# Performance work log

Hardware: AMD Instinct MI355X
Metric: run time of the kernel (lower is better)

## Reference

```python
import jax, jax.numpy as jnp
import numpy as np
from jax import lax

LN_EPS = 1e-6  # flax LayerNorm default


def _layernorm(x, scale, bias):
    mu = jnp.mean(x, axis=-1, keepdims=True)
    var = jnp.mean(jnp.square(x - mu), axis=-1, keepdims=True)
    return (x - mu) * lax.rsqrt(var + LN_EPS) * scale + bias


def _lstm_layer(c0, h0, Wi, Wh, b, x):
    # x: [B, T, F]; carry c/h: [B, H]; gate order i, f, g, o (flax)
    def step(carry, xt):
        c, h = carry
        z = xt @ Wi + h @ Wh + b  # [B, 4H]
        i, f, g, o = jnp.split(z, 4, axis=-1)
        i = jax.nn.sigmoid(i); f = jax.nn.sigmoid(f)
        g = jnp.tanh(g); o = jax.nn.sigmoid(o)
        c = f * c + i * g
        h = o * jnp.tanh(c)
        return (c, h), h
    (cT, hT), hs = lax.scan(step, (c0, h0), jnp.swapaxes(x, 0, 1))
    return cT, hT, jnp.swapaxes(hs, 0, 1)  # hs: [B, T, H]


def setup_inputs() -> dict:
    key = jax.random.key(0)
    ks = jax.random.split(key, 16)
    B, T, F, H, P, A = 64, 128, 512, 1024, 1024, 32
    s = 0.05
    return {
        "x": jax.random.normal(ks[0], (B, T, F), jnp.float32),
        "c0": jnp.zeros((2, B, H), jnp.float32),
        "h0": jnp.zeros((2, B, H), jnp.float32),
        "W_pre": jax.random.normal(ks[1], (F, P), jnp.float32) * s,
        "b_pre": jnp.zeros((P,), jnp.float32),
        "ln_scale": jnp.ones((P,), jnp.float32),
        "ln_bias": jnp.zeros((P,), jnp.float32),
        "Wi0": jax.random.normal(ks[2], (P, 4 * H), jnp.float32) * s,
        "Wh0": jax.random.normal(ks[3], (H, 4 * H), jnp.float32) * s,
        "b0": jnp.zeros((4 * H,), jnp.float32),
        "Wi1": jax.random.normal(ks[4], (H, 4 * H), jnp.float32) * s,
        "Wh1": jax.random.normal(ks[5], (H, 4 * H), jnp.float32) * s,
        "b1": jnp.zeros((4 * H,), jnp.float32),
        "W_post": jax.random.normal(ks[6], (H, P), jnp.float32) * s,
        "b_post": jnp.zeros((P,), jnp.float32),
        "W_out": jax.random.normal(ks[7], (P, A), jnp.float32) * s,
        "b_out": jnp.zeros((A,), jnp.float32),
        "training": False,
    }


def reference(x, c0, h0, W_pre, b_pre, ln_scale, ln_bias,
              Wi0, Wh0, b0, Wi1, Wh1, b1,
              W_post, b_post, W_out, b_out, training):
    # preprocessing: Dense -> LayerNorm -> relu
    h = jax.nn.relu(_layernorm(x @ W_pre + b_pre, ln_scale, ln_bias))
    # two stacked LSTM layers scanned over time
    c1, h1, h = _lstm_layer(c0[0], h0[0], Wi0, Wh0, b0, h)
    c2, h2, h = _lstm_layer(c0[1], h0[1], Wi1, Wh1, b1, h)
    # postprocessing: Dense -> relu (dropout deterministic => identity)
    h = jax.nn.relu(h @ W_post + b_post)
    logits = h @ W_out + b_out  # [B, T, action_dim]
    new_carry = (jnp.stack([c1, c2]), jnp.stack([h1, h2]))
    return new_carry, logits
```

## Files before the change

kernel.cpp:

```cpp
#include <hip/hip_runtime.h>
#include <hip/hip_bf16.h>
#include <math.h>

typedef __attribute__((ext_vector_type(8))) short short8;
typedef __attribute__((ext_vector_type(4))) float f32x4;
typedef __attribute__((ext_vector_type(4))) unsigned u32x4;
typedef unsigned short u16;
typedef unsigned long long u64;

__device__ __forceinline__ u16 f2bf(float f) {
    union { float f; unsigned u; } v; v.f = f;
    unsigned r = v.u + 0x7fffu + ((v.u >> 16) & 1u);
    return (u16)(r >> 16);
}
__device__ __forceinline__ float bf2f(u16 b) {
    union { unsigned u; float f; } v; v.u = ((unsigned)b) << 16;
    return v.f;
}
__device__ __forceinline__ float fast_sigmoid(float x) {
    return __builtin_amdgcn_rcpf(1.f + __expf(-x));
}
__device__ __forceinline__ float fast_tanh(float x) {
    return 1.f - 2.f * __builtin_amdgcn_rcpf(1.f + __expf(2.f * x));
}
__device__ __forceinline__ u32x4 ldg16(const void* p) {
    u32x4 r;
    asm volatile("global_load_dwordx4 %0, %1, off"
                 : "=v"(r) : "v"(p) : "memory");
    return r;
}

__device__ __forceinline__ void tr_tile(const float* __restrict__ W,
                                        u16* __restrict__ WT, int K, int N,
                                        int bid, int tid, float (*tile)[33]) {
    int gx = N >> 5;
    int bx = bid % gx, by = bid / gx;
    int n0 = bx * 32, k0 = by * 32;
    int tx = tid & 31, ty = tid >> 5;
    #pragma unroll
    for (int j = 0; j < 32; j += 8)
        tile[ty + j][tx] = W[(size_t)(k0 + ty + j) * N + n0 + tx];
    __syncthreads();
    #pragma unroll
    for (int j = 0; j < 32; j += 8)
        WT[(size_t)(n0 + ty + j) * K + k0 + tx] = f2bf(tile[tx][ty + j]);
}

__global__ __launch_bounds__(256) void k_prep(
    const float* __restrict__ x, u16* __restrict__ Xb,
    const float* __restrict__ h0, u16* __restrict__ hs0, u16* __restrict__ hs1,
    unsigned* __restrict__ ctr,
    const float* __restrict__ Wpre, u16* __restrict__ WTpre,
    const float* __restrict__ Wi0, u16* __restrict__ WTi0,
    const float* __restrict__ Wh0, u16* __restrict__ WTh0,
    const float* __restrict__ Wi1, u16* __restrict__ WTi1,
    const float* __restrict__ Wh1, u16* __restrict__ WTh1,
    const float* __restrict__ Wpost, u16* __restrict__ WTpost,
    const float* __restrict__ Wout, u16* __restrict__ WTout) {
    __shared__ float tile[32][33];
    int bid = blockIdx.x, tid = threadIdx.x;
    if (bid == 0) {
        for (int i = tid; i < 4096; i += 256) ctr[i] = 0u;
        return;
    }
    bid -= 1;
    if (bid < 16384) {
        int i = bid * 256 + tid;
        Xb[i] = f2bf(x[i]);
        return;
    }
    bid -= 16384;
    if (bid < 512) {
        int i = bid * 256 + tid;
        int layer = i >> 16, j = i & 65535;
        int b = j >> 10, jj = j & 1023;
        u16 v = f2bf(h0[(size_t)layer * 65536 + j]);
        u16* dst = layer ? hs1 : hs0;
        dst[(size_t)(jj >> 3) * 512 + b * 8 + (jj & 7)] = v;
        return;
    }
    bid -= 512;
    if (bid < 512)  { tr_tile(Wpre,  WTpre,  512,  1024, bid, tid, tile); return; }
    bid -= 512;
    if (bid < 4096) { tr_tile(Wi0,   WTi0,   1024, 4096, bid, tid, tile); return; }
    bid -= 4096;
    if (bid < 4096) { tr_tile(Wh0,   WTh0,   1024, 4096, bid, tid, tile); return; }
    bid -= 4096;
    if (bid < 4096) { tr_tile(Wi1,   WTi1,   1024, 4096, bid, tid, tile); return; }
    bid -= 4096;
    if (bid < 4096) { tr_tile(Wh1,   WTh1,   1024, 4096, bid, tid, tile); return; }
    bid -= 4096;
    if (bid < 1024) { tr_tile(Wpost, WTpost, 1024, 1024, bid, tid, tile); return; }
    bid -= 1024;
    tr_tile(Wout, WTout, 1024, 32, bid, tid, tile);
}
#define PREP_BLOCKS (1 + 16384 + 512 + 512 + 4 * 4096 + 1024 + 32)

template <int MODE>
__global__ __launch_bounds__(256) void k_gemm(const u16* __restrict__ A,
                                              const u16* __restrict__ BT,
                                              const float* __restrict__ bias,
                                              void* __restrict__ Cout,
                                              int M, int N, int K) {
    const int w = threadIdx.x >> 6, l = threadIdx.x & 63;
    const int lm = l & 15, lq = l >> 4;
    const int r0 = blockIdx.y * 64 + w * 16;
    const int c0 = blockIdx.x * 64;
    const u16* arow = A + (size_t)(r0 + lm) * K + lq * 8;
    const u16* bp0 = BT + (size_t)(c0 + lm) * K + lq * 8;
    const u16* bp1 = bp0 + (size_t)16 * K;
    const u16* bp2 = bp0 + (size_t)32 * K;
    const u16* bp3 = bp0 + (size_t)48 * K;
    f32x4 acc0 = {0.f, 0.f, 0.f, 0.f}, acc1 = acc0, acc2 = acc0, acc3 = acc0;
    for (int k0 = 0; k0 < K; k0 += 32) {
        short8 a = *(const short8*)(arow + k0);
        acc0 = __builtin_amdgcn_mfma_f32_16x16x32_bf16(a, *(const short8*)(bp0 + k0), acc0, 0, 0, 0);
        acc1 = __builtin_amdgcn_mfma_f32_16x16x32_bf16(a, *(const short8*)(bp1 + k0), acc1, 0, 0, 0);
        acc2 = __builtin_amdgcn_mfma_f32_16x16x32_bf16(a, *(const short8*)(bp2 + k0), acc2, 0, 0, 0);
        acc3 = __builtin_amdgcn_mfma_f32_16x16x32_bf16(a, *(const short8*)(bp3 + k0), acc3, 0, 0, 0);
    }
    f32x4 accs[4] = {acc0, acc1, acc2, acc3};
    #pragma unroll
    for (int nt = 0; nt < 4; nt++) {
        #pragma unroll
        for (int r = 0; r < 4; r++) {
            int row = r0 + lq * 4 + r;
            int col = c0 + nt * 16 + lm;
            float v = accs[nt][r] + bias[col];
            if (MODE == 0) {
                ((float*)Cout)[(size_t)row * N + col] = v;
            } else {
                if (MODE == 2) v = fmaxf(v, 0.f);
                ((u16*)Cout)[(size_t)row * N + col] = f2bf(v);
            }
        }
    }
}

__global__ __launch_bounds__(256) void k_ln_relu(const float* __restrict__ X,
                                                 const float* __restrict__ scale,
                                                 const float* __restrict__ bias,
                                                 u16* __restrict__ preS) {
    const int N = 1024;
    int row = blockIdx.x;
    int b = row >> 7, t = row & 127;
    const float* x = X + (size_t)row * N;
    __shared__ float vbuf[1024];
    float s = 0.f, ss = 0.f;
    float vals[4];
    #pragma unroll
    for (int j = 0; j < 4; j++) {
        float v = x[threadIdx.x + 256 * j];
        vals[j] = v; s += v; ss += v * v;
    }
    #pragma unroll
    for (int o = 32; o > 0; o >>= 1) { s += __shfl_down(s, o); ss += __shfl_down(ss, o); }
    __shared__ float rs[4], rss[4];
    int w = threadIdx.x >> 6;
    if ((threadIdx.x & 63) == 0) { rs[w] = s; rss[w] = ss; }
    __syncthreads();
    __shared__ float smu, sinv;
    if (threadIdx.x == 0) {
        float a = rs[0] + rs[1] + rs[2] + rs[3];
        float bq = rss[0] + rss[1] + rss[2] + rss[3];
        float mu = a * (1.f / N);
        float var = bq * (1.f / N) - mu * mu;
        smu = mu; sinv = rsqrtf(var + 1e-6f);
    }
    __syncthreads();
    float mu = smu, inv = sinv;
    #pragma unroll
    for (int j = 0; j < 4; j++) {
        int i = threadIdx.x + 256 * j;
        float v = (vals[j] - mu) * inv * scale[i] + bias[i];
        vbuf[i] = fmaxf(v, 0.f);
    }
    __syncthreads();
    if (threadIdx.x < 128) {
        int g = threadIdx.x;
        union { u16 h[8]; u32x4 v; } pk;
        #pragma unroll
        for (int e = 0; e < 8; e++) pk.h[e] = f2bf(vbuf[g * 8 + e]);
        *(u32x4*)(preS + (size_t)t * 65536 + (size_t)g * 512 + b * 8) = pk.v;
    }
}

#define FBLOCKS 256
__global__ __launch_bounds__(512, 1) void k_lstm_fused(
    const u16* __restrict__ WiT0, const u16* __restrict__ WhT0,
    const u16* __restrict__ WiT1, const u16* __restrict__ WhT1,
    const u16* __restrict__ preS, const float* __restrict__ b0v,
    const float* __restrict__ b1v, const float* __restrict__ c0_all,
    u16* __restrict__ hs0, u16* __restrict__ hs1, u16* __restrict__ Hp,
    float* __restrict__ out, unsigned* __restrict__ ctr) {
    const int bk = blockIdx.x;
    const int role = bk >> 7;
    const int bkl = bk & 127;
    const int tid = threadIdx.x;
    const int w = tid >> 6, l = tid & 63, lm = l & 15, lq = l >> 4;
    const int kp = w >> 2, rt = w & 3;

    __shared__ u16 whs[65536];
    __shared__ float zbuf[2 * 64 * 33];
    __shared__ int gflag[2];

    {
        const u16* Wx = role ? WiT1 : WiT0;
        const u16* Wh = role ? WhT1 : WhT0;
        for (int f = tid; f < 8192; f += 512) {
            int flm = f & 15, flq = (f >> 4) & 3;
            int fi = (f >> 6) & 31;
            int rest = f >> 11;
            int fg = rest & 1, fkp = (rest >> 1) & 1;
            int lc = fg * 16 + flm;
            int gcolw = (lc >> 3) * 1024 + bkl * 8 + (lc & 7);
            int k = fi * 32 + flq * 8;
            const u16* src = (fkp == 0 ? Wx : Wh) + (size_t)gcolw * 1024 + k;
            *(short8*)(whs + (size_t)f * 8) = *(const short8*)src;
        }
    }
    if (tid == 0) { gflag[0] = -1; gflag[1] = -1; }
    const int u = tid & 7, b = tid >> 3;
    const int gcol = bkl * 8 + u;
    float c = (c0_all + (size_t)role * 65536)[(size_t)b * 1024 + gcol];
    const float* bv = role ? b1v : b0v;
    float bi0 = bv[gcol], bi1 = bv[1024 + gcol];
    float bi2 = bv[2048 + gcol], bi3 = bv[3072 + gcol];
    u16* hs_my = role ? hs1 : hs0;
    float* c_out = out + (size_t)role * 65536;
    float* h_out = out + 131072 + (size_t)role * 65536;
    const int lanoff = (lq * 16 + lm) * 8;
    __syncthreads();

    for (int t = 0; t < 128; t++) {
        if (role || kp == 1) {
            int need = (role && kp == 0) ? t + 1 : t;
            if (rt == 0) {
                if (need > 0) {
                    int cbase = (role && kp) ? 128 : 0;
                    for (;;) {
                        unsigned a0 = __hip_atomic_load(&ctr[(cbase + l) * 16], __ATOMIC_RELAXED,
                                                        __HIP_MEMORY_SCOPE_AGENT);
                        unsigned a1 = __hip_atomic_load(&ctr[(cbase + 64 + l) * 16], __ATOMIC_RELAXED,
                                                        __HIP_MEMORY_SCOPE_AGENT);
                        if (__all((a0 >= (unsigned)need) && (a1 >= (unsigned)need))) break;
                        __builtin_amdgcn_s_sleep(1);
                    }
                }
                __hip_atomic_store(&gflag[kp], need, __ATOMIC_RELAXED,
                                   __HIP_MEMORY_SCOPE_WORKGROUP);
            } else {
                while (__hip_atomic_load(&gflag[kp], __ATOMIC_RELAXED,
                                         __HIP_MEMORY_SCOPE_WORKGROUP) < need)
                    __builtin_amdgcn_s_sleep(1);
            }
        }

        const u16* abase;
        if (!role) abase = (kp == 0) ? preS + (size_t)t * 65536
                                     : hs0 + (size_t)t * 65536;
        else       abase = (kp == 0) ? hs0 + (size_t)(t + 1) * 65536
                                     : hs1 + (size_t)t * 65536;
        const u16* arow = abase + (size_t)lq * 512 + (rt * 16 + lm) * 8;
        const u16* bw0 = whs + kp * 32768 + lanoff;

        f32x4 zv = {0.f, 0.f, 0.f, 0.f};
        f32x4 ac0[4] = {zv, zv, zv, zv}, ac1[4] = {zv, zv, zv, zv};
        #define STEPF(Ai, i)                                                      \
        {   union { u32x4 q; short8 v; } _a; _a.q = (Ai);                         \
            short8 _b0 = *(const short8*)(bw0 + (i) * 512);                       \
            short8 _b1 = *(const short8*)(bw0 + 16384 + (i) * 512);               \
            ac0[(i) & 3] = __builtin_amdgcn_mfma_f32_16x16x32_bf16(_a.v, _b0, ac0[(i) & 3], 0, 0, 0); \
            ac1[(i) & 3] = __builtin_amdgcn_mfma_f32_16x16x32_bf16(_a.v, _b1, ac1[(i) & 3], 0, 0, 0); }

        u32x4 A0 = ldg16(arow +     0), A1 = ldg16(arow +  2048);
        u32x4 A2 = ldg16(arow +  4096), A3 = ldg16(arow +  6144);
        u32x4 A4 = ldg16(arow +  8192), A5 = ldg16(arow + 10240);
        u32x4 A6 = ldg16(arow + 12288), A7 = ldg16(arow + 14336);
        u32x4 A8 = ldg16(arow + 16384), A9 = ldg16(arow + 18432);
        u32x4 A10 = ldg16(arow + 20480), A11 = ldg16(arow + 22528);
        u32x4 A12 = ldg16(arow + 24576), A13 = ldg16(arow + 26624);
        u32x4 A14 = ldg16(arow + 28672), A15 = ldg16(arow + 30720);
        u32x4 A16 = ldg16(arow + 32768), A17 = ldg16(arow + 34816);
        u32x4 A18 = ldg16(arow + 36864), A19 = ldg16(arow + 38912);
        u32x4 A20 = ldg16(arow + 40960), A21 = ldg16(arow + 43008);
        u32x4 A22 = ldg16(arow + 45056), A23 = ldg16(arow + 47104);
        u32x4 A24 = ldg16(arow + 49152), A25 = ldg16(arow + 51200);
        u32x4 A26 = ldg16(arow + 53248), A27 = ldg16(arow + 55296);
        u32x4 A28 = ldg16(arow + 57344), A29 = ldg16(arow + 59392);
        u32x4 A30 = ldg16(arow + 61440), A31 = ldg16(arow + 63488);
        asm volatile("s_waitcnt vmcnt(24)"
                     : "+v"(A0), "+v"(A1), "+v"(A2), "+v"(A3),
                       "+v"(A4), "+v"(A5), "+v"(A6), "+v"(A7) :: "memory");
        STEPF(A0, 0) STEPF(A1, 1) STEPF(A2, 2) STEPF(A3, 3)
        STEPF(A4, 4) STEPF(A5, 5) STEPF(A6, 6) STEPF(A7, 7)
        asm volatile("s_waitcnt vmcnt(16)"
                     : "+v"(A8), "+v"(A9), "+v"(A10), "+v"(A11),
                       "+v"(A12), "+v"(A13), "+v"(A14), "+v"(A15) :: "memory");
        STEPF(A8, 8) STEPF(A9, 9) STEPF(A10, 10) STEPF(A11, 11)
        STEPF(A12, 12) STEPF(A13, 13) STEPF(A14, 14) STEPF(A15, 15)
        asm volatile("s_waitcnt vmcnt(8)"
                     : "+v"(A16), "+v"(A17), "+v"(A18), "+v"(A19),
                       "+v"(A20), "+v"(A21), "+v"(A22), "+v"(A23) :: "memory");
        STEPF(A16, 16) STEPF(A17, 17) STEPF(A18, 18) STEPF(A19, 19)
        STEPF(A20, 20) STEPF(A21, 21) STEPF(A22, 22) STEPF(A23, 23)
        asm volatile("s_waitcnt vmcnt(0)"
                     : "+v"(A24), "+v"(A25), "+v"(A26), "+v"(A27),
                       "+v"(A28), "+v"(A29), "+v"(A30), "+v"(A31) :: "memory");
        STEPF(A24, 24) STEPF(A25, 25) STEPF(A26, 26) STEPF(A27, 27)
        STEPF(A28, 28) STEPF(A29, 29) STEPF(A30, 30) STEPF(A31, 31)
        #undef STEPF
        f32x4 acc0 = (ac0[0] + ac0[1]) + (ac0[2] + ac0[3]);
        f32x4 acc1 = (ac1[0] + ac1[1]) + (ac1[2] + ac1[3]);

        {
            float* zb = zbuf + (size_t)kp * 2112;
            #pragma unroll
            for (int r = 0; r < 4; r++) {
                int row = rt * 16 + lq * 4 + r;
                zb[row * 33 + lm] = acc0[r];
                zb[row * 33 + 16 + lm] = acc1[r];
            }
        }
        __syncthreads();

        {
            const float* z0 = zbuf + (size_t)b * 33;
            const float* z1 = z0 + 2112;
            float gi = z0[u]      + z1[u]      + bi0;
            float gf = z0[8 + u]  + z1[8 + u]  + bi1;
            float gg = z0[16 + u] + z1[16 + u] + bi2;
            float go = z0[24 + u] + z1[24 + u] + bi3;
            gi = fast_sigmoid(gi);
            gf = fast_sigmoid(gf);
            gg = fast_tanh(gg);
            go = fast_sigmoid(go);
            c = gf * c + gi * gg;
            float h = go * fast_tanh(c);
            unsigned hv = (unsigned)f2bf(h);
            int base = l & 56;
            unsigned p0 = __shfl(hv, base + 0, 64) | (__shfl(hv, base + 1, 64) << 16);
            unsigned p1 = __shfl(hv, base + 2, 64) | (__shfl(hv, base + 3, 64) << 16);
            unsigned p2 = __shfl(hv, base + 4, 64) | (__shfl(hv, base + 5, 64) << 16);
            unsigned p3 = __shfl(hv, base + 6, 64) | (__shfl(hv, base + 7, 64) << 16);
            if (u == 0) {
                u32x4 pv = {p0, p1, p2, p3};
                u16* dst = hs_my + (size_t)(t + 1) * 65536 + (size_t)bkl * 512 + b * 8;
                asm volatile("global_store_dwordx4 %0, %1, off sc0 sc1"
                             :: "v"(dst), "v"(pv) : "memory");
                if (role) {
                    u16* d2 = Hp + (size_t)(t * 64 + b) * 1024 + bkl * 8;
                    *(u32x4*)d2 = pv;
                }
            }
            if (t == 127) {
                c_out[(size_t)b * 1024 + gcol] = c;
                h_out[(size_t)b * 1024 + gcol] = h;
            }
        }
        __syncthreads();

        if (tid == 0)
            __hip_atomic_store(&ctr[bk * 16], (unsigned)(t + 1), __ATOMIC_RELAXED,
                               __HIP_MEMORY_SCOPE_AGENT);
    }
}

__global__ __launch_bounds__(256) void k_logits(const u16* __restrict__ Pact,
                                                const u16* __restrict__ WoT,
                                                const float* __restrict__ bout,
                                                float* __restrict__ out) {
    int r = blockIdx.x * 8 + (threadIdx.x >> 5);
    int n = threadIdx.x & 31;
    const u16* a = Pact + (size_t)r * 1024;
    const u16* wv = WoT + (size_t)n * 1024;
    float s = 0.f;
    for (int k = 0; k < 1024; k += 8) {
        short8 av = *(const short8*)(a + k);
        short8 wvv = *(const short8*)(wv + k);
        #pragma unroll
        for (int j = 0; j < 8; j++)
            s += bf2f((u16)av[j]) * bf2f((u16)wvv[j]);
    }
    int t = r >> 6, b = r & 63;
    out[((size_t)b * 128 + t) * 32 + n] = s + bout[n];
}

extern "C" void kernel_launch(void* const* d_in, const int* in_sizes, int n_in,
                              void* d_out, int out_size, void* d_ws, size_t ws_size,
                              hipStream_t stream) {
    const float* x      = (const float*)d_in[0];
    const float* c0     = (const float*)d_in[1];
    const float* h0     = (const float*)d_in[2];
    const float* W_pre  = (const float*)d_in[3];
    const float* b_pre  = (const float*)d_in[4];
    const float* ln_s   = (const float*)d_in[5];
    const float* ln_b   = (const float*)d_in[6];
    const float* Wi0    = (const float*)d_in[7];
    const float* Wh0    = (const float*)d_in[8];
    const float* b0     = (const float*)d_in[9];
    const float* Wi1    = (const float*)d_in[10];
    const float* Wh1    = (const float*)d_in[11];
    const float* b1     = (const float*)d_in[12];
    const float* W_post = (const float*)d_in[13];
    const float* b_post = (const float*)d_in[14];
    const float* W_out  = (const float*)d_in[15];
    const float* b_out  = (const float*)d_in[16];
    float* out = (float*)d_out;

    char* ws = (char*)d_ws;
    size_t off = 0;
    auto alloc = [&](size_t bytes) {
        void* p = ws + off;
        off += (bytes + 255) & ~(size_t)255;
        return p;
    };
    u16* WTpre  = (u16*)alloc((size_t)1024 * 512 * 2);
    u16* WTi0   = (u16*)alloc((size_t)4096 * 1024 * 2);
    u16* WTh0   = (u16*)alloc((size_t)4096 * 1024 * 2);
    u16* WTi1   = (u16*)alloc((size_t)4096 * 1024 * 2);
    u16* WTh1   = (u16*)alloc((size_t)4096 * 1024 * 2);
    u16* WTpost = (u16*)alloc((size_t)1024 * 1024 * 2);
    u16* WTout  = (u16*)alloc((size_t)32 * 1024 * 2);
    u16* Xb     = (u16*)alloc((size_t)8192 * 512 * 2);
    u16* preS   = (u16*)alloc((size_t)128 * 65536 * 2);
    u16* hs0    = (u16*)alloc((size_t)129 * 65536 * 2);
    u16* hs1    = (u16*)alloc((size_t)129 * 65536 * 2);
    u16* postact= (u16*)alloc((size_t)8192 * 1024 * 2);
    unsigned* ctr = (unsigned*)alloc(32768);
    void* unionreg = alloc((size_t)8192 * 4096 * 2);
    float* pre_f32 = (float*)unionreg;
    u16* Hplain = (u16*)unionreg;

    k_prep<<<PREP_BLOCKS, 256, 0, stream>>>(
        x, Xb, h0, hs0, hs1, ctr,
        W_pre, WTpre, Wi0, WTi0, Wh0, WTh0, Wi1, WTi1, Wh1, WTh1,
        W_post, WTpost, W_out, WTout);

    k_gemm<0><<<dim3(16, 128), 256, 0, stream>>>(Xb, WTpre, b_pre, pre_f32, 8192, 1024, 512);
    k_ln_relu<<<8192, 256, 0, stream>>>(pre_f32, ln_s, ln_b, preS);

    {
        const u16* WiT0_ = WTi0; const u16* WhT0_ = WTh0;
        const u16* WiT1_ = WTi1; const u16* WhT1_ = WTh1;
        const u16* preS_ = preS; const float* b0_ = b0; const float* b1_ = b1;
        const float* c0_ = c0; u16* hs0_ = hs0; u16* hs1_ = hs1;
        u16* Hp_ = Hplain; float* out_ = out; unsigned* ctr_ = ctr;
        void* args[] = {&WiT0_, &WhT0_, &WiT1_, &WhT1_, &preS_, &b0_, &b1_,
                        &c0_, &hs0_, &hs1_, &Hp_, &out_, &ctr_};
        hipLaunchCooperativeKernel((void*)k_lstm_fused, dim3(FBLOCKS), dim3(512),
                                   args, 0, stream);
    }

    k_gemm<2><<<dim3(16, 128), 256, 0, stream>>>(Hplain, WTpost, b_post, postact,
                                                 8192, 1024, 1024);
    k_logits<<<1024, 256, 0, stream>>>(postact, WTout, b_out, out + 262144);
}
```

Baseline: 1.102 ms.

## Fuse pre-GEMM, LayerNorm, LSTM and post-processing into one cooperative kernel

Moves the input Dense plus LayerNorm+ReLU, the two-layer LSTM recurrence and the post Dense+ReLU and logits into a single cooperative persistent kernel of 256 blocks. A global counter barrier separates the preprocessing phase from the recurrence. This removes several kernel launches and the fp32 intermediate round-trip through global memory. The trade-off is that the pre-GEMM now runs on only 256 blocks instead of a wide grid, and the post stages are likewise confined to the persistent grid, so those phases may be less parallel. The shown recurrence also drops the 4-way split accumulators that the old kernel used.

```diff
diff --git a/kernel.cpp b/kernel.cpp
--- a/kernel.cpp
+++ b/kernel.cpp
@@ -6,7 +6,6 @@
 typedef __attribute__((ext_vector_type(4))) float f32x4;
 typedef __attribute__((ext_vector_type(4))) unsigned u32x4;
 typedef unsigned short u16;
-typedef unsigned long long u64;
 
 __device__ __forceinline__ u16 f2bf(float f) {
     union { float f; unsigned u; } v; v.f = f;
@@ -28,6 +27,10 @@
     asm volatile("global_load_dwordx4 %0, %1, off"
                  : "=v"(r) : "v"(p) : "memory");
     return r;
+}
+__device__ __forceinline__ void stg16sc(void* p, u32x4 v) {
+    asm volatile("global_store_dwordx4 %0, %1, off sc0 sc1"
+                 :: "v"(p), "v"(v) : "memory");
 }
 
 __device__ __forceinline__ void tr_tile(const float* __restrict__ W,
@@ -60,7 +63,7 @@
     __shared__ float tile[32][33];
     int bid = blockIdx.x, tid = threadIdx.x;
     if (bid == 0) {
-        for (int i = tid; i < 4096; i += 256) ctr[i] = 0u;
+        for (int i = tid; i < 8192; i += 256) ctr[i] = 0u;
         return;
     }
     bid -= 1;
@@ -96,294 +99,324 @@
 }
 #define PREP_BLOCKS (1 + 16384 + 512 + 512 + 4 * 4096 + 1024 + 32)
 
-template <int MODE>
-__global__ __launch_bounds__(256) void k_gemm(const u16* __restrict__ A,
-                                              const u16* __restrict__ BT,
-                                              const float* __restrict__ bias,
-                                              void* __restrict__ Cout,
-                                              int M, int N, int K) {
-    const int w = threadIdx.x >> 6, l = threadIdx.x & 63;
-    const int lm = l & 15, lq = l >> 4;
-    const int r0 = blockIdx.y * 64 + w * 16;
-    const int c0 = blockIdx.x * 64;
-    const u16* arow = A + (size_t)(r0 + lm) * K + lq * 8;
-    const u16* bp0 = BT + (size_t)(c0 + lm) * K + lq * 8;
-    const u16* bp1 = bp0 + (size_t)16 * K;
-    const u16* bp2 = bp0 + (size_t)32 * K;
-    const u16* bp3 = bp0 + (size_t)48 * K;
-    f32x4 acc0 = {0.f, 0.f, 0.f, 0.f}, acc1 = acc0, acc2 = acc0, acc3 = acc0;
-    for (int k0 = 0; k0 < K; k0 += 32) {
-        short8 a = *(const short8*)(arow + k0);
-        acc0 = __builtin_amdgcn_mfma_f32_16x16x32_bf16(a, *(const short8*)(bp0 + k0), acc0, 0, 0, 0);
-        acc1 = __builtin_amdgcn_mfma_f32_16x16x32_bf16(a, *(const short8*)(bp1 + k0), acc1, 0, 0, 0);
-        acc2 = __builtin_amdgcn_mfma_f32_16x16x32_bf16(a, *(const short8*)(bp2 + k0), acc2, 0, 0, 0);
-        acc3 = __builtin_amdgcn_mfma_f32_16x16x32_bf16(a, *(const short8*)(bp3 + k0), acc3, 0, 0, 0);
-    }
-    f32x4 accs[4] = {acc0, acc1, acc2, acc3};
-    #pragma unroll
-    for (int nt = 0; nt < 4; nt++) {
-        #pragma unroll
-        for (int r = 0; r < 4; r++) {
-            int row = r0 + lq * 4 + r;
-            int col = c0 + nt * 16 + lm;
-            float v = accs[nt][r] + bias[col];
-            if (MODE == 0) {
-                ((float*)Cout)[(size_t)row * N + col] = v;
-            } else {
-                if (MODE == 2) v = fmaxf(v, 0.f);
-                ((u16*)Cout)[(size_t)row * N + col] = f2bf(v);
-            }
-        }
-    }
-}
-
-__global__ __launch_bounds__(256) void k_ln_relu(const float* __restrict__ X,
-                                                 const float* __restrict__ scale,
-                                                 const float* __restrict__ bias,
-                                                 u16* __restrict__ preS) {
-    const int N = 1024;
-    int row = blockIdx.x;
-    int b = row >> 7, t = row & 127;
-    const float* x = X + (size_t)row * N;
-    __shared__ float vbuf[1024];
-    float s = 0.f, ss = 0.f;
-    float vals[4];
-    #pragma unroll
-    for (int j = 0; j < 4; j++) {
-        float v = x[threadIdx.x + 256 * j];
-        vals[j] = v; s += v; ss += v * v;
-    }
-    #pragma unroll
-    for (int o = 32; o > 0; o >>= 1) { s += __shfl_down(s, o); ss += __shfl_down(ss, o); }
-    __shared__ float rs[4], rss[4];
-    int w = threadIdx.x >> 6;
-    if ((threadIdx.x & 63) == 0) { rs[w] = s; rss[w] = ss; }
-    __syncthreads();
-    __shared__ float smu, sinv;
-    if (threadIdx.x == 0) {
-        float a = rs[0] + rs[1] + rs[2] + rs[3];
-        float bq = rss[0] + rss[1] + rss[2] + rss[3];
-        float mu = a * (1.f / N);
-        float var = bq * (1.f / N) - mu * mu;
-        smu = mu; sinv = rsqrtf(var + 1e-6f);
-    }
-    __syncthreads();
-    float mu = smu, inv = sinv;
-    #pragma unroll
-    for (int j = 0; j < 4; j++) {
-        int i = threadIdx.x + 256 * j;
-        float v = (vals[j] - mu) * inv * scale[i] + bias[i];
-        vbuf[i] = fmaxf(v, 0.f);
-    }
-    __syncthreads();
-    if (threadIdx.x < 128) {
-        int g = threadIdx.x;
-        union { u16 h[8]; u32x4 v; } pk;
-        #pragma unroll
-        for (int e = 0; e < 8; e++) pk.h[e] = f2bf(vbuf[g * 8 + e]);
-        *(u32x4*)(preS + (size_t)t * 65536 + (size_t)g * 512 + b * 8) = pk.v;
-    }
-}
-
 #define FBLOCKS 256
-__global__ __launch_bounds__(512, 1) void k_lstm_fused(
+__global__ __launch_bounds__(512, 1) void k_fused_all(
+    const u16* __restrict__ Xb, const u16* __restrict__ WTpre,
+    const float* __restrict__ b_pre, const float* __restrict__ ln_s,
+    const float* __restrict__ ln_b,
     const u16* __restrict__ WiT0, const u16* __restrict__ WhT0,
     const u16* __restrict__ WiT1, const u16* __restrict__ WhT1,
-    const u16* __restrict__ preS, const float* __restrict__ b0v,
+    u16* __restrict__ preS, const float* __restrict__ b0v,
     const float* __restrict__ b1v, const float* __restrict__ c0_all,
     u16* __restrict__ hs0, u16* __restrict__ hs1, u16* __restrict__ Hp,
+    const u16* __restrict__ WTpost, const float* __restrict__ b_post,
+    const u16* __restrict__ WTout, const float* __restrict__ b_out,
     float* __restrict__ out, unsigned* __restrict__ ctr) {
     const int bk = blockIdx.x;
     const int role = bk >> 7;
     const int bkl = bk & 127;
     const int tid = threadIdx.x;
     const int w = tid >> 6, l = tid & 63, lm = l & 15, lq = l >> 4;
-    const int kp = w >> 2, rt = w & 3;
 
     __shared__ u16 whs[65536];
     __shared__ float zbuf[2 * 64 * 33];
     __shared__ int gflag[2];
 
     {
-        const u16* Wx = role ? WiT1 : WiT0;
-        const u16* Wh = role ? WhT1 : WhT0;
-        for (int f = tid; f < 8192; f += 512) {
-            int flm = f & 15, flq = (f >> 4) & 3;
-            int fi = (f >> 6) & 31;
-            int rest = f >> 11;
-            int fg = rest & 1, fkp = (rest >> 1) & 1;
-            int lc = fg * 16 + flm;
-            int gcolw = (lc >> 3) * 1024 + bkl * 8 + (lc & 7);
-            int k = fi * 32 + flq * 8;
-            const u16* src = (fkp == 0 ? Wx : Wh) + (size_t)gcolw * 1024 + k;
-            *(short8*)(whs + (size_t)f * 8) = *(const short8*)src;
+        float* zout = (float*)whs;
+        float* lnstat = zbuf;
+        for (int p = 0; p < 2; p++) {
+            int R0 = bk * 32 + p * 16;
+            #pragma unroll
+            for (int ct = 0; ct < 2; ct++) {
+                int c0 = w * 128 + ct * 64;
+                const u16* arow = Xb + (size_t)(R0 + lm) * 512 + lq * 8;
+                const u16* bp0 = WTpre + (size_t)(c0 + lm) * 512 + lq * 8;
+                const u16* bp1 = bp0 + 16 * 512;
+                const u16* bp2 = bp0 + 32 * 512;
+                const u16* bp3 = bp0 + 48 * 512;
+                f32x4 a0 = {0.f, 0.f, 0.f, 0.f}, a1 = a0, a2 = a0, a3 = a0;
+                for (int k0 = 0; k0 < 512; k0 += 32) {
+                    short8 a = *(const short8*)(arow + k0);
+                    a0 = __builtin_amdgcn_mfma_f32_16x16x32_bf16(a, *(const short8*)(bp0 + k0), a0, 0, 0, 0);
+                    a1 = __builtin_amdgcn_mfma_f32_16x16x32_bf16(a, *(const short8*)(bp1 + k0), a1, 0, 0, 0);
+                    a2 = __builtin_amdgcn_mfma_f32_16x16x32_bf16(a, *(const short8*)(bp2 + k0), a2, 0, 0, 0);
+                    a3 = __builtin_amdgcn_mfma_f32_16x16x32_bf16(a, *(const short8*)(bp3 + k0), a3, 0, 0, 0);
+                }
+                f32x4 accs[4] = {a0, a1, a2, a3};
+                #pragma unroll
+                for (int nt = 0; nt < 4; nt++) {
+                    #pragma unroll
+                    for (int r = 0; r < 4; r++) {
+                        int col = c0 + nt * 16 + lm;
+                        zout[(lq * 4 + r) * 1036 + col] = accs[nt][r] + b_pre[col];
+                    }
+                }
+            }
+            __syncthreads();
+            {
+                int row = tid >> 5, tr = tid & 31;
+                float s = 0.f, ss = 0.f;
+                #pragma unroll
+                for (int j = 0; j < 32; j++) {
+                    float v = zout[row * 1036 + tr + j * 32];
+                    s += v; ss += v * v;
+                }
+                #pragma unroll
+                for (int o = 16; o > 0; o >>= 1) {
+                    s += __shfl_down(s, o, 32);
+                    ss += __shfl_down(ss, o, 32);
+                }
+                if (tr == 0) {
+                    float mu = s * (1.f / 1024.f);
+                    float var = ss * (1.f / 1024.f) - mu * mu;
+                    lnstat[row * 2] = mu;
+                    lnstat[row * 2 + 1] = rsqrtf(var + 1e-6f);
+                }
+            }
+            __syncthreads();
+            {
+                int row = tid >> 5, tr = tid & 31;
+                int R = R0 + row, bb = R >> 7, t = R & 127;
+                float mu = lnstat[row * 2], inv = lnstat[row * 2 + 1];
+                #pragma unroll
+                for (int j = 0; j < 4; j++) {
+                    int g = tr + j * 32;
+                    union { u16 h[8]; u32x4 v; } pk;
+                    #pragma unroll
+                    for (int e = 0; e < 8; e++) {
+                        int col = g * 8 + e;
+                        float v = (zout[row * 1036 + col] - mu) * inv * ln_s[col] + ln_b[col];
+                        pk.h[e] = f2bf(fmaxf(v, 0.f));
+                    }
+                    stg16sc(preS + (size_t)t * 65536 + (size_t)g * 512 + bb * 8, pk.v);
+                }
+            }
+            __syncthreads();
         }
     }
-    if (tid == 0) { gflag[0] = -1; gflag[1] = -1; }
-    const int u = tid & 7, b = tid >> 3;
-    const int gcol = bkl * 8 + u;
-    float c = (c0_all + (size_t)role * 65536)[(size_t)b * 1024 + gcol];
-    const float* bv = role ? b1v : b0v;
-    float bi0 = bv[gcol], bi1 = bv[1024 + gcol];
-    float bi2 = bv[2048 + gcol], bi3 = bv[3072 + gcol];
-    u16* hs_my = role ? hs1 : hs0;
-    float* c_out = out + (size_t)role * 65536;
-    float* h_out = out + 131072 + (size_t)role * 65536;
-    const int lanoff = (lq * 16 + lm) * 8;
     __syncthreads();
-
-    for (int t = 0; t < 128; t++) {
-        if (role || kp == 1) {
-            int need = (role && kp == 0) ? t + 1 : t;
-            if (rt == 0) {
-                if (need > 0) {
-                    int cbase = (role && kp) ? 128 : 0;
-                    for (;;) {
-                        unsigned a0 = __hip_atomic_load(&ctr[(cbase + l) * 16], __ATOMIC_RELAXED,
-                                                        __HIP_MEMORY_SCOPE_AGENT);
-                        unsigned a1 = __hip_atomic_load(&ctr[(cbase + 64 + l) * 16], __ATOMIC_RELAXED,
-                                                        __HIP_MEMORY_SCOPE_AGENT);
-                        if (__all((a0 >= (unsigned)need) && (a1 >= (unsigned)need))) break;
+    if (tid == 0) {
+        __hip_atomic_fetch_add(&ctr[4096], 1u, __ATOMIC_ACQ_REL, __HIP_MEMORY_SCOPE_AGENT);
+        while (__hip_atomic_load(&ctr[4096], __ATOMIC_ACQUIRE, __HIP_MEMORY_SCOPE_AGENT) < (unsigned)FBLOCKS)
+            __builtin_amdgcn_s_sleep(2);
+    }
+    __syncthreads();
+
+    {
+        const int kp = w >> 2, rt = w & 3;
+        {
+            const u16* Wx = role ? WiT1 : WiT0;
+            const u16* Wh = role ? WhT1 : WhT0;
+            for (int f = tid; f < 8192; f += 512) {
+                int flm = f & 15, flq = (f >> 4) & 3;
+                int fi = (f >> 6) & 31;
+                int rest = f >> 11;
+                int fg = rest & 1, fkp = (rest >> 1) & 1;
+                int lc = fg * 16 + flm;
+                int gcolw = (lc >> 3) * 1024 + bkl * 8 + (lc & 7);
+                int k = fi * 32 + flq * 8;
+                const u16* src = (fkp == 0 ? Wx : Wh) + (size_t)gcolw * 1024 + k;
+                *(short8*)(whs + (size_t)f * 8) = *(const short8*)src;
+            }
+        }
+        if (tid == 0) { gflag[0] = -1; gflag[1] = -1; }
+        const int u = tid & 7, b = tid >> 3;
+        const int gcol = bkl * 8 + u;
+        float c = (c0_all + (size_t)role * 65536)[(size_t)b * 1024 + gcol];
+        const float* bv = role ? b1v : b0v;
+        float bi0 = bv[gcol], bi1 = bv[1024 + gcol];
+        float bi2 = bv[2048 + gcol], bi3 = bv[3072 + gcol];
+        u16* hs_my = role ? hs1 : hs0;
+        float* c_out = out + (size_t)role * 65536;
+        float* h_out = out + 131072 + (size_t)role * 65536;
+        const int lanoff = (lq * 16 + lm) * 8;
+        __syncthreads();
+
+        for (int t = 0; t < 128; t++) {
+            if (role || kp == 1) {
+                int need = (role && kp == 0) ? t + 1 : t;
+                if (rt == 0) {
+                    if (need > 0) {
+                        int cbase = (role && kp) ? 128 : 0;
+                        for (;;) {
+                            unsigned a0 = __hip_atomic_load(&ctr[(cbase + l) * 16], __ATOMIC_RELAXED,
+                                                            __HIP_MEMORY_SCOPE_AGENT);
+                            unsigned a1 = __hip_atomic_load(&ctr[(cbase + 64 + l) * 16], __ATOMIC_RELAXED,
+                                                            __HIP_MEMORY_SCOPE_AGENT);
+                            if (__all((a0 >= (unsigned)need) && (a1 >= (unsigned)need))) break;
+                            __builtin_amdgcn_s_sleep(1);
+                        }
+                    }
+                    __hip_atomic_store(&gflag[kp], need, __ATOMIC_RELAXED,
+                                       __HIP_MEMORY_SCOPE_WORKGROUP);
+                } else {
+                    while (__hip_atomic_load(&gflag[kp], __ATOMIC_RELAXED,
+                                             __HIP_MEMORY_SCOPE_WORKGROUP) < need)
                         __builtin_amdgcn_s_sleep(1);
+                }
+            }
+
+            const u16* abase;
+            if (!role) abase = (kp == 0) ? preS + (size_t)t * 65536
+                                         : hs0 + (size_t)t * 65536;
+            else       abase = (kp == 0) ? hs0 + (size_t)(t + 1) * 65536
+                                         : hs1 + (size_t)t * 65536;
+            const u16* arow = abase + (size_t)lq * 512 + (rt * 16 + lm) * 8;
+            const u16* bw0 = whs + kp * 32768 + lanoff;
+
+            f32x4 acc0 = {0.f, 0.f, 0.f, 0.f}, acc1 = acc0;
+            #define STEPF(Ai, i)                                                      \
+            {   union { u32x4 q; short8 v; } _a; _a.q = (Ai);                         \
+                short8 _b0 = *(const short8*)(bw0 + (i) * 512);                       \
+                short8 _b1 = *(const short8*)(bw0 + 16384 + (i) * 512);               \
+                acc0 = __builtin_amdgcn_mfma_f32_16x16x32_bf16(_a.v, _b0, acc0, 0, 0, 0); \
+                acc1 = __builtin_amdgcn_mfma_f32_16x16x32_bf16(_a.v, _b1, acc1, 0, 0, 0); }
+
+            u32x4 A0 = ldg16(arow +     0), A1 = ldg16(arow +  2048);
+            u32x4 A2 = ldg16(arow +  4096), A3 = ldg16(arow +  6144);
+            u32x4 A4 = ldg16(arow +  8192), A5 = ldg16(arow + 10240);
+            u32x4 A6 = ldg16(arow + 12288), A7 = ldg16(arow + 14336);
+            u32x4 A8 = ldg16(arow + 16384), A9 = ldg16(arow + 18432);
+            u32x4 A10 = ldg16(arow + 20480), A11 = ldg16(arow + 22528);
+            u32x4 A12 = ldg16(arow + 24576), A13 = ldg16(arow + 26624);
+            u32x4 A14 = ldg16(arow + 28672), A15 = ldg16(arow + 30720);
+            u32x4 A16 = ldg16(arow + 32768), A17 = ldg16(arow + 34816);
+            u32x4 A18 = ldg16(arow + 36864), A19 = ldg16(arow + 38912);
+            u32x4 A20 = ldg16(arow + 40960), A21 = ldg16(arow + 43008);
+            u32x4 A22 = ldg16(arow + 45056), A23 = ldg16(arow + 47104);
+            u32x4 A24 = ldg16(arow + 49152), A25 = ldg16(arow + 51200);
+            u32x4 A26 = ldg16(arow + 53248), A27 = ldg16(arow + 55296);
+            u32x4 A28 = ldg16(arow + 57344), A29 = ldg16(arow + 59392);
+            u32x4 A30 = ldg16(arow + 61440), A31 = ldg16(arow + 63488);
+            asm volatile("s_waitcnt vmcnt(24)"
+                         : "+v"(A0), "+v"(A1), "+v"(A2), "+v"(A3),
+                           "+v"(A4), "+v"(A5), "+v"(A6), "+v"(A7) :: "memory");
+            STEPF(A0, 0) STEPF(A1, 1) STEPF(A2, 2) STEPF(A3, 3)
+            STEPF(A4, 4) STEPF(A5, 5) STEPF(A6, 6) STEPF(A7, 7)
+            asm volatile("s_waitcnt vmcnt(16)"
+                         : "+v"(A8), "+v"(A9), "+v"(A10), "+v"(A11),
+                           "+v"(A12), "+v"(A13), "+v"(A14), "+v"(A15) :: "memory");
+            STEPF(A8, 8) STEPF(A9, 9) STEPF(A10, 10) STEPF(A11, 11)
+            STEPF(A12, 12) STEPF(A13, 13) STEPF(A14, 14) STEPF(A15, 15)
+            asm volatile("s_waitcnt vmcnt(8)"
+                         : "+v"(A16), "+v"(A17), "+v"(A18), "+v"(A19),
+                           "+v"(A20), "+v"(A21), "+v"(A22), "+v"(A23) :: "memory");
+            STEPF(A16, 16) STEPF(A17, 17) STEPF(A18, 18) STEPF(A19, 19)
+            STEPF(A20, 20) STEPF(A21, 21) STEPF(A22, 22) STEPF(A23, 23)
+            asm volatile("s_waitcnt vmcnt(0)"
+                         : "+v"(A24), "+v"(A25), "+v"(A26), "+v"(A27),
+                           "+v"(A28), "+v"(A29), "+v"(A30), "+v"(A31) :: "memory");
+            STEPF(A24, 24) STEPF(A25, 25) STEPF(A26, 26) STEPF(A27, 27)
+            STEPF(A28, 28) STEPF(A29, 29) STEPF(A30, 30) STEPF(A31, 31)
+            #undef STEPF
+
+            {
+                float* zb = zbuf + (size_t)kp * 2112;
+                #pragma unroll
+                for (int r = 0; r < 4; r++) {
+                    int row = rt * 16 + lq * 4 + r;
+                    zb[row * 33 + lm] = acc0[r];
+                    zb[row * 33 + 16 + lm] = acc1[r];
+                }
+            }
+            __syncthreads();
+
+            {
+                const float* z0 = zbuf + (size_t)b * 33;
+                const float* z1 = z0 + 2112;
+                float gi = z0[u]      + z1[u]      + bi0;
+                float gf = z0[8 + u]  + z1[8 + u]  + bi1;
+                float gg = z0[16 + u] + z1[16 + u] + bi2;
+                float go = z0[24 + u] + z1[24 + u] + bi3;
+                gi = fast_sigmoid(gi);
+                gf = fast_sigmoid(gf);
+                gg = fast_tanh(gg);
+                go = fast_sigmoid(go);
+                c = gf * c + gi * gg;
+                float h = go * fast_tanh(c);
+                unsigned hv = (unsigned)f2bf(h);
+                int base = l & 56;
+                unsigned p0 = __shfl(hv, base + 0, 64) | (__shfl(hv, base + 1, 64) << 16);
+                unsigned p1 = __shfl(hv, base + 2, 64) | (__shfl(hv, base + 3, 64) << 16);
+                unsigned p2 = __shfl(hv, base + 4, 64) | (__shfl(hv, base + 5, 64) << 16);
+                unsigned p3 = __shfl(hv, base + 6, 64) | (__shfl(hv, base + 7, 64) << 16);
+                if (u == 0) {
+                    u32x4 pv = {p0, p1, p2, p3};
+                    stg16sc(hs_my + (size_t)(t + 1) * 65536 + (size_t)bkl * 512 + b * 8, pv);
+                    if (role)
+                        stg16sc(Hp + (size_t)(t * 64 + b) * 1024 + bkl * 8, pv);
+                }
+                if (t == 127) {
+                    c_out[(size_t)b * 1024 + gcol] = c;
+                    h_out[(size_t)b * 1024 + gcol] = h;
+                }
+            }
+            __syncthreads();
+
+            if (tid == 0)
+                __hip_atomic_store(&ctr[bk * 16], (unsigned)(t + 1), __ATOMIC_RELAXED,
+                                   __HIP_MEMORY_SCOPE_AGENT);
+        }
+    }
+    __syncthreads();
+    if (tid == 0) {
+        __hip_atomic_fetch_add(&ctr[4160], 1u, __ATOMIC_ACQ_REL, __HIP_MEMORY_SCOPE_AGENT);
+        while (__hip_atomic_load(&ctr[4160], __ATOMIC_ACQUIRE, __HIP_MEMORY_SCOPE_AGENT) < (unsigned)FBLOCKS)
+            __builtin_amdgcn_s_sleep(2);
+    }
+    __syncthreads();
+
+    {
+        u16* pact = whs;
+        for (int p = 0; p < 2; p++) {
+            int R0 = bk * 32 + p * 16;
+            #pragma unroll
+            for (int ct = 0; ct < 2; ct++) {
+                int c0 = w * 128 + ct * 64;
+                const u16* arow = Hp + (size_t)(R0 + lm) * 1024 + lq * 8;
+                const u16* bp0 = WTpost + (size_t)(c0 + lm) * 1024 + lq * 8;
+                const u16* bp1 = bp0 + 16 * 1024;
+                const u16* bp2 = bp0 + 32 * 1024;
+                const u16* bp3 = bp0 + 48 * 1024;
+                f32x4 a0 = {0.f, 0.f, 0.f, 0.f}, a1 = a0, a2 = a0, a3 = a0;
+                for (int k0 = 0; k0 < 1024; k0 += 32) {
+                    short8 a = *(const short8*)(arow + k0);
+                    a0 = __builtin_amdgcn_mfma_f32_16x16x32_bf16(a, *(const short8*)(bp0 + k0), a0, 0, 0, 0);
+                    a1 = __builtin_amdgcn_mfma_f32_16x16x32_bf16(a, *(const short8*)(bp1 + k0), a1, 0, 0, 0);
+                    a2 = __builtin_amdgcn_mfma_f32_16x16x32_bf16(a, *(const short8*)(bp2 + k0), a2, 0, 0, 0);
+                    a3 = __builtin_amdgcn_mfma_f32_16x16x32_bf16(a, *(const short8*)(bp3 + k0), a3, 0, 0, 0);
+                }
+                f32x4 accs[4] = {a0, a1, a2, a3};
+                #pragma unroll
+                for (int nt = 0; nt < 4; nt++) {
+                    #pragma unroll
+                    for (int r = 0; r < 4; r++) {
+                        int col = c0 + nt * 16 + lm;
+                        float v = accs[nt][r] + b_post[col];
+                        pact[(lq * 4 + r) * 1040 + col] = f2bf(fmaxf(v, 0.f));
                     }
                 }
-                __hip_atomic_store(&gflag[kp], need, __ATOMIC_RELAXED,
-                                   __HIP_MEMORY_SCOPE_WORKGROUP);
-            } else {
-                while (__hip_atomic_load(&gflag[kp], __ATOMIC_RELAXED,
-                                         __HIP_MEMORY_SCOPE_WORKGROUP) < need)
-                    __builtin_amdgcn_s_sleep(1);
-            }
+            }
+            __syncthreads();
+            {
+                int row = tid >> 5, n = tid & 31;
+                const u16* av = pact + row * 1040;
+                const u16* wv = WTout + (size_t)n * 1024;
+                float s = 0.f;
+                for (int k = 0; k < 1024; k += 8) {
+                    short8 a8 = *(const short8*)(av + k);
+                    short8 w8 = *(const short8*)(wv + k);
+                    #pragma unroll
+                    for (int jj = 0; jj < 8; jj++)
+                        s += bf2f((u16)a8[jj]) * bf2f((u16)w8[jj]);
+                }
+                int R = R0 + row, t = R >> 6, bb = R & 63;
+                out[262144 + ((size_t)bb * 128 + t) * 32 + n] = s + b_out[n];
+            }
+            __syncthreads();
         }
-
-        const u16* abase;
-        if (!role) abase = (kp == 0) ? preS + (size_t)t * 65536
-                                     : hs0 + (size_t)t * 65536;
-        else       abase = (kp == 0) ? hs0 + (size_t)(t + 1) * 65536
-                                     : hs1 + (size_t)t * 65536;
-        const u16* arow = abase + (size_t)lq * 512 + (rt * 16 + lm) * 8;
-        const u16* bw0 = whs + kp * 32768 + lanoff;
-
-        f32x4 zv = {0.f, 0.f, 0.f, 0.f};
-        f32x4 ac0[4] = {zv, zv, zv, zv}, ac1[4] = {zv, zv, zv, zv};
-        #define STEPF(Ai, i)                                                      \
-        {   union { u32x4 q; short8 v; } _a; _a.q = (Ai);                         \
-            short8 _b0 = *(const short8*)(bw0 + (i) * 512);                       \
-            short8 _b1 = *(const short8*)(bw0 + 16384 + (i) * 512);               \
-            ac0[(i) & 3] = __builtin_amdgcn_mfma_f32_16x16x32_bf16(_a.v, _b0, ac0[(i) & 3], 0, 0, 0); \
-            ac1[(i) & 3] = __builtin_amdgcn_mfma_f32_16x16x32_bf16(_a.v, _b1, ac1[(i) & 3], 0, 0, 0); }
-
-        u32x4 A0 = ldg16(arow +     0), A1 = ldg16(arow +  2048);
-        u32x4 A2 = ldg16(arow +  4096), A3 = ldg16(arow +  6144);
-        u32x4 A4 = ldg16(arow +  8192), A5 = ldg16(arow + 10240);
-        u32x4 A6 = ldg16(arow + 12288), A7 = ldg16(arow + 14336);
-        u32x4 A8 = ldg16(arow + 16384), A9 = ldg16(arow + 18432);
-        u32x4 A10 = ldg16(arow + 20480), A11 = ldg16(arow + 22528);
-        u32x4 A12 = ldg16(arow + 24576), A13 = ldg16(arow + 26624);
-        u32x4 A14 = ldg16(arow + 28672), A15 = ldg16(arow + 30720);
-        u32x4 A16 = ldg16(arow + 32768), A17 = ldg16(arow + 34816);
-        u32x4 A18 = ldg16(arow + 36864), A19 = ldg16(arow + 38912);
-        u32x4 A20 = ldg16(arow + 40960), A21 = ldg16(arow + 43008);
-        u32x4 A22 = ldg16(arow + 45056), A23 = ldg16(arow + 47104);
-        u32x4 A24 = ldg16(arow + 49152), A25 = ldg16(arow + 51200);
-        u32x4 A26 = ldg16(arow + 53248), A27 = ldg16(arow + 55296);
-        u32x4 A28 = ldg16(arow + 57344), A29 = ldg16(arow + 59392);
-        u32x4 A30 = ldg16(arow + 61440), A31 = ldg16(arow + 63488);
-        asm volatile("s_waitcnt vmcnt(24)"
-                     : "+v"(A0), "+v"(A1), "+v"(A2), "+v"(A3),
-                       "+v"(A4), "+v"(A5), "+v"(A6), "+v"(A7) :: "memory");
-        STEPF(A0, 0) STEPF(A1, 1) STEPF(A2, 2) STEPF(A3, 3)
-        STEPF(A4, 4) STEPF(A5, 5) STEPF(A6, 6) STEPF(A7, 7)
-        asm volatile("s_waitcnt vmcnt(16)"
-                     : "+v"(A8), "+v"(A9), "+v"(A10), "+v"(A11),
-                       "+v"(A12), "+v"(A13), "+v"(A14), "+v"(A15) :: "memory");
-        STEPF(A8, 8) STEPF(A9, 9) STEPF(A10, 10) STEPF(A11, 11)
-        STEPF(A12, 12) STEPF(A13, 13) STEPF(A14, 14) STEPF(A15, 15)
-        asm volatile("s_waitcnt vmcnt(8)"
-                     : "+v"(A16), "+v"(A17), "+v"(A18), "+v"(A19),
-                       "+v"(A20), "+v"(A21), "+v"(A22), "+v"(A23) :: "memory");
-        STEPF(A16, 16) STEPF(A17, 17) STEPF(A18, 18) STEPF(A19, 19)
-        STEPF(A20, 20) STEPF(A21, 21) STEPF(A22, 22) STEPF(A23, 23)
-        asm volatile("s_waitcnt vmcnt(0)"
-                     : "+v"(A24), "+v"(A25), "+v"(A26), "+v"(A27),
-                       "+v"(A28), "+v"(A29), "+v"(A30), "+v"(A31) :: "memory");
-        STEPF(A24, 24) STEPF(A25, 25) STEPF(A26, 26) STEPF(A27, 27)
-        STEPF(A28, 28) STEPF(A29, 29) STEPF(A30, 30) STEPF(A31, 31)
-        #undef STEPF
-        f32x4 acc0 = (ac0[0] + ac0[1]) + (ac0[2] + ac0[3]);
-        f32x4 acc1 = (ac1[0] + ac1[1]) + (ac1[2] + ac1[3]);
-
-        {
-            float* zb = zbuf + (size_t)kp * 2112;
-            #pragma unroll
-            for (int r = 0; r < 4; r++) {
-                int row = rt * 16 + lq * 4 + r;
-                zb[row * 33 + lm] = acc0[r];
-                zb[row * 33 + 16 + lm] = acc1[r];
-            }
-        }
-        __syncthreads();
-
-        {
-            const float* z0 = zbuf + (size_t)b * 33;
-            const float* z1 = z0 + 2112;
-            float gi = z0[u]      + z1[u]      + bi0;
-            float gf = z0[8 + u]  + z1[8 + u]  + bi1;
-            float gg = z0[16 + u] + z1[16 + u] + bi2;
-            float go = z0[24 + u] + z1[24 + u] + bi3;
-            gi = fast_sigmoid(gi);
-            gf = fast_sigmoid(gf);
-            gg = fast_tanh(gg);
-            go = fast_sigmoid(go);
-            c = gf * c + gi * gg;
-            float h = go * fast_tanh(c);
-            unsigned hv = (unsigned)f2bf(h);
-            int base = l & 56;
-            unsigned p0 = __shfl(hv, base + 0, 64) | (__shfl(hv, base + 1, 64) << 16);
-            unsigned p1 = __shfl(hv, base + 2, 64) | (__shfl(hv, base + 3, 64) << 16);
-            unsigned p2 = __shfl(hv, base + 4, 64) | (__shfl(hv, base + 5, 64) << 16);
-            unsigned p3 = __shfl(hv, base + 6, 64) | (__shfl(hv, base + 7, 64) << 16);
-            if (u == 0) {
-                u32x4 pv = {p0, p1, p2, p3};
-                u16* dst = hs_my + (size_t)(t + 1) * 65536 + (size_t)bkl * 512 + b * 8;
-                asm volatile("global_store_dwordx4 %0, %1, off sc0 sc1"
-                             :: "v"(dst), "v"(pv) : "memory");
-                if (role) {
-                    u16* d2 = Hp + (size_t)(t * 64 + b) * 1024 + bkl * 8;
-                    *(u32x4*)d2 = pv;
-                }
-            }
-            if (t == 127) {
-                c_out[(size_t)b * 1024 + gcol] = c;
-                h_out[(size_t)b * 1024 + gcol] = h;
-            }
-        }
-        __syncthreads();
-
-        if (tid == 0)
-            __hip_atomic_store(&ctr[bk * 16], (unsigned)(t + 1), __ATOMIC_RELAXED,
-                               __HIP_MEMORY_SCOPE_AGENT);
-    }
-}
-
-__global__ __launch_bounds__(256) void k_logits(const u16* __restrict__ Pact,
-                                                const u16* __restrict__ WoT,
-                                                const float* __restrict__ bout,
-                                                float* __restrict__ out) {
-    int r = blockIdx.x * 8 + (threadIdx.x >> 5);
-    int n = threadIdx.x & 31;
-    const u16* a = Pact + (size_t)r * 1024;
-    const u16* wv = WoT + (size_t)n * 1024;
-    float s = 0.f;
-    for (int k = 0; k < 1024; k += 8) {
-        short8 av = *(const short8*)(a + k);
-        short8 wvv = *(const short8*)(wv + k);
-        #pragma unroll
-        for (int j = 0; j < 8; j++)
-            s += bf2f((u16)av[j]) * bf2f((u16)wvv[j]);
-    }
-    int t = r >> 6, b = r & 63;
-    out[((size_t)b * 128 + t) * 32 + n] = s + bout[n];
+    }
 }
 
 extern "C" void kernel_launch(void* const* d_in, const int* in_sizes, int n_in,
@@ -426,33 +459,29 @@
     u16* preS   = (u16*)alloc((size_t)128 * 65536 * 2);
     u16* hs0    = (u16*)alloc((size_t)129 * 65536 * 2);
     u16* hs1    = (u16*)alloc((size_t)129 * 65536 * 2);
-    u16* postact= (u16*)alloc((size_t)8192 * 1024 * 2);
     unsigned* ctr = (unsigned*)alloc(32768);
-    void* unionreg = alloc((size_t)8192 * 4096 * 2);
-    float* pre_f32 = (float*)unionreg;
-    u16* Hplain = (u16*)unionreg;
+    u16* Hplain = (u16*)alloc((size_t)8192 * 1024 * 2);
 
     k_prep<<<PREP_BLOCKS, 256, 0, stream>>>(
         x, Xb, h0, hs0, hs1, ctr,
         W_pre, WTpre, Wi0, WTi0, Wh0, WTh0, Wi1, WTi1, Wh1, WTh1,
         W_post, WTpost, W_out, WTout);
 
-    k_gemm<0><<<dim3(16, 128), 256, 0, stream>>>(Xb, WTpre, b_pre, pre_f32, 8192, 1024, 512);
-    k_ln_relu<<<8192, 256, 0, stream>>>(pre_f32, ln_s, ln_b, preS);
-
     {
+        const u16* Xb_ = Xb; const u16* WTpre_ = WTpre;
+        const float* bpre_ = b_pre; const float* lns_ = ln_s; const float* lnb_ = ln_b;
         const u16* WiT0_ = WTi0; const u16* WhT0_ = WTh0;
         const u16* WiT1_ = WTi1; const u16* WhT1_ = WTh1;
-        const u16* preS_ = preS; const float* b0_ = b0; const float* b1_ = b1;
-        const float* c0_ = c0; u16* hs0_ = hs0; u16* hs1_ = hs1;
-        u16* Hp_ = Hplain; float* out_ = out; unsigned* ctr_ = ctr;
-        void* args[] = {&WiT0_, &WhT0_, &WiT1_, &WhT1_, &preS_, &b0_, &b1_,
-                        &c0_, &hs0_, &hs1_, &Hp_, &out_, &ctr_};
-        hipLaunchCooperativeKernel((void*)k_lstm_fused, dim3(FBLOCKS), dim3(512),
+        u16* preS_ = preS; const float* b0_ = b0; const float* b1_ = b1;
+        const float* c0_ = c0; u16* hs0_ = hs0; u16* hs1_ = hs1; u16* Hp_ = Hplain;
+        const u16* WTpost_ = WTpost; const float* bpost_ = b_post;
+        const u16* WTout_ = WTout; const float* bout_ = b_out;
+        float* out_ = out; unsigned* ctr_ = ctr;
+        void* args[] = {&Xb_, &WTpre_, &bpre_, &lns_, &lnb_,
+                        &WiT0_, &WhT0_, &WiT1_, &WhT1_,
+                        &preS_, &b0_, &b1_, &c0_, &hs0_, &hs1_, &Hp_,
+                        &WTpost_, &bpost_, &WTout_, &bout_, &out_, &ctr_};
+        hipLaunchCooperativeKernel((void*)k_fused_all, dim3(FBLOCKS), dim3(512),
                                    args, 0, stream);
     }
-
-    k_gemm<2><<<dim3(16, 128), 256, 0, stream>>>(Hplain, WTpost, b_post, postact,
-                                                 8192, 1024, 1024);
-    k_logits<<<1024, 256, 0, stream>>>(postact, WTout, b_out, out + 262144);
-}
+}
```

Result: slower. 1.707 ms (+55.0%).
